# Performance work log

Measured on AMD Instinct MI355X. Metric: run time of the kernel, lower is better.

Reference implementation:

```python
import jax, jax.numpy as jnp
import numpy as np

EPS = 1e-6
H = 8  # num_heads

def setup_inputs() -> dict:
    key = jax.random.key(0)
    ks = jax.random.split(key, 8)
    B, N, M, C, L = 4, 8192, 2048, 512, 256
    s = lambda f_in: 1.0 / np.sqrt(f_in)
    return {
        "input_tokens": jax.random.normal(ks[0], (B, N, C), jnp.float32),
        "query_tokens": jax.random.normal(ks[1], (B, M, C), jnp.float32),
        "Wq": jax.random.normal(ks[2], (C, L), jnp.float32) * s(C),
        "bq": jax.random.normal(ks[3], (L,), jnp.float32) * 0.01,
        "Wk": jax.random.normal(ks[4], (C, L), jnp.float32) * s(C),
        "bk": jax.random.normal(ks[5], (L,), jnp.float32) * 0.01,
        "Wv": jax.random.normal(ks[6], (C, C), jnp.float32) * s(C),
        "bv": jax.random.normal(ks[7], (C,), jnp.float32) * 0.01,
    }

def reference(input_tokens, query_tokens, Wq, bq, Wk, bk, Wv, bv):
    B, N, C = input_tokens.shape
    _, M, _ = query_tokens.shape
    L = Wq.shape[1]
    dL, dC = L // H, C // H
    # projections + head split
    q = (query_tokens @ Wq + bq).reshape(B, M, H, dL)
    k = (input_tokens @ Wk + bk).reshape(B, N, H, dL)
    v = (input_tokens @ Wv + bv).reshape(B, N, H, dC)
    # ELU+1 feature maps (positive kernel)
    q = jax.nn.elu(q) + 1.0
    k = jax.nn.elu(k) + 1.0
    # kv aggregation over input tokens: [B,H,dC,dL]
    kv = jnp.einsum('bnhd,bnhm->bhmd', k, v)
    # normalizer: q . sum_n k  -> [B,M,H]
    z = 1.0 / (jnp.einsum('bmhd,bhd->bmh', q, k.sum(axis=1)) + EPS)
    out = jnp.einsum('bmhd,bhcd,bmh->bmhc', q, kv, z)  # [B,M,H,dC]
    return out.reshape(B, M, C)
```

## Files before the change

### kernel.cpp

```cpp
#include <hip/hip_runtime.h>
#include <hip/hip_bf16.h>
#include <stdint.h>

typedef __bf16 bf16x8 __attribute__((ext_vector_type(8)));
typedef float f32x4 __attribute__((ext_vector_type(4)));

#define GLD16(gp, lp) __builtin_amdgcn_global_load_lds( \
    (__attribute__((address_space(1))) void*)(gp),      \
    (__attribute__((address_space(3))) void*)(lp), 16, 0, 0)

#define Bb 4
#define Nn 8192
#define Mm 2048
#define Cc 512
#define Ll 256
#define Hh 8
#define NTOK 32768

__global__ __launch_bounds__(256) void convert_q(
    const float* __restrict__ Q, __hip_bfloat16* __restrict__ Qb)
{
    long i = ((long)blockIdx.x * 256 + threadIdx.x) * 8;
    float4 a = *(const float4*)(Q + i);
    float4 b = *(const float4*)(Q + i + 4);
    __hip_bfloat16 t8[8] = {
        __float2bfloat16(a.x), __float2bfloat16(a.y),
        __float2bfloat16(a.z), __float2bfloat16(a.w),
        __float2bfloat16(b.x), __float2bfloat16(b.y),
        __float2bfloat16(b.z), __float2bfloat16(b.w)};
    *(uint4*)(Qb + i) = *(const uint4*)t8;
}

__global__ __launch_bounds__(256) void transpose_x(
    const float* __restrict__ X,
    __hip_bfloat16* __restrict__ Xb, __hip_bfloat16* __restrict__ XbT)
{
    __shared__ __hip_bfloat16 ldsT[64][72];
    const int tn = blockIdx.x, tc = blockIdx.y;
    const long n0 = (long)tn * 64;
    const int c0 = tc * 64;
    const int t = threadIdx.x;
    const int rl = t >> 4;
    const int c4 = (t & 15) * 4;
#pragma unroll
    for (int u = 0; u < 4; ++u) {
        const int row = rl + u * 16;
        f32x4 a = *(const f32x4*)(X + (n0 + row) * Cc + c0 + c4);
        __hip_bfloat16 b4[4] = {
            __float2bfloat16(a.x), __float2bfloat16(a.y),
            __float2bfloat16(a.z), __float2bfloat16(a.w)};
        *(ushort2*)(&Xb[(n0 + row) * Cc + c0 + c4]) = *(const ushort2*)b4;
        *(ushort2*)(&Xb[(n0 + row) * Cc + c0 + c4 + 2]) = *(const ushort2*)(b4 + 2);
#pragma unroll
        for (int i = 0; i < 4; ++i) ldsT[c4 + i][row] = b4[i];
    }
    __syncthreads();
#pragma unroll
    for (int u = 0; u < 2; ++u) {
        const int v = u * 256 + t;
        const int orow = v >> 3;
        const int oc8 = (v & 7) * 8;
        bf16x8 r = *(const bf16x8*)(&ldsT[orow][oc8]);
        *(bf16x8*)(&XbT[(long)(c0 + orow) * NTOK + n0 + oc8]) = r;
    }
}

__global__ __launch_bounds__(256) void transpose_w2(
    const float* __restrict__ Wk, const float* __restrict__ Wq,
    __hip_bfloat16* __restrict__ WkT, __hip_bfloat16* __restrict__ WqT)
{
    int idx = blockIdx.x * 256 + threadIdx.x;
    const int NK = 256 * 512;
    if (idx < NK) {
        int j = idx >> 9, c = idx & 511;
        WkT[idx] = __float2bfloat16(Wk[c * 256 + j]);
    } else {
        int k = idx - NK;
        int j = k >> 9, c = k & 511;
        WqT[k] = __float2bfloat16(Wq[c * 256 + j]);
    }
}

template<int MODE>
__global__ __launch_bounds__(256)
void gemm_bt(const __hip_bfloat16* __restrict__ A, long lda,
             const __hip_bfloat16* __restrict__ Bt, long ldb,
             const float* __restrict__ bias,
             void* __restrict__ Cout, long ldc, int Klen)
{
    __shared__ char lds[2][16384];
    const int tid  = threadIdx.x;
    const int lane = tid & 63;
    const int wv   = tid >> 6;
    const int wm   = wv >> 1, wn = wv & 1;
    const long gm0 = (long)blockIdx.x * 128;
    const long gn0 = (long)blockIdx.y * 128;

    long koff_el = 0;
    if (MODE == 2) {
        const int z = blockIdx.z;
        koff_el = (long)(z >> 3) * Nn + (long)(z & 7) * 1024;
    }

    const int o0 = tid * 16;
    const int row0 = o0 >> 6;
    const int kb0 = o0 & 63;
    const int o1 = o0 + 4096;
    const int row1 = row0 + 64;
    const long sA = lda * 2, sB = ldb * 2;
    const char* pA0 = (const char*)A + (gm0 + row0) * sA + koff_el * 2 + kb0;
    const char* pA1 = (const char*)A + (gm0 + row1) * sA + koff_el * 2 + kb0;
    const char* pB0 = (const char*)Bt + (gn0 + row0) * sB + koff_el * 2 + kb0;
    const char* pB1 = (const char*)Bt + (gn0 + row1) * sB + koff_el * 2 + kb0;

    f32x4 acc[4][4];
#pragma unroll
    for (int i = 0; i < 4; i++)
#pragma unroll
        for (int j = 0; j < 4; j++) acc[i][j] = (f32x4){0.f, 0.f, 0.f, 0.f};

    const int l16 = lane & 15, lq = lane >> 4;
    int aoff[4], boff[4];
#pragma unroll
    for (int i = 0; i < 4; i++) {
        aoff[i] = (wm * 64 + i * 16 + l16) * 64 + lq * 16;
        boff[i] = 8192 + (wn * 64 + i * 16 + l16) * 64 + lq * 16;
    }

    const int KT = Klen >> 5;
    {
        char* bf = lds[0];
        GLD16(pA0, bf + o0); GLD16(pA1, bf + o1);
        GLD16(pB0, bf + 8192 + o0); GLD16(pB1, bf + 8192 + o1);
    }
    __syncthreads();
    for (int kt = 0; kt < KT; ++kt) {
        const int cur = kt & 1;
        if (kt + 1 < KT) {
            char* bf = lds[cur ^ 1];
            const long kb = (long)(kt + 1) * 64;
            GLD16(pA0 + kb, bf + o0); GLD16(pA1 + kb, bf + o1);
            GLD16(pB0 + kb, bf + 8192 + o0); GLD16(pB1 + kb, bf + 8192 + o1);
        }
        const char* lp = lds[cur];
        bf16x8 af[4], bfr[4];
#pragma unroll
        for (int i = 0; i < 4; i++) af[i]  = *(const bf16x8*)(lp + aoff[i]);
#pragma unroll
        for (int j = 0; j < 4; j++) bfr[j] = *(const bf16x8*)(lp + boff[j]);
#pragma unroll
        for (int i = 0; i < 4; i++)
#pragma unroll
            for (int j = 0; j < 4; j++)
                acc[i][j] = __builtin_amdgcn_mfma_f32_16x16x32_bf16(
                    af[i], bfr[j], acc[i][j], 0, 0, 0);
        __syncthreads();
    }

    __hip_bfloat16* Cb = (__hip_bfloat16*)Cout;
    float* Cf = (float*)Cout;
    if (MODE == 2) Cf += (long)blockIdx.z * (512 * 256);
#pragma unroll
    for (int i = 0; i < 4; i++) {
        const long gmr = gm0 + wm * 64 + i * 16 + lq * 4;
#pragma unroll
        for (int j = 0; j < 4; j++) {
            const int gn = (int)gn0 + wn * 64 + j * 16 + l16;
#pragma unroll
            for (int v = 0; v < 4; v++) {
                float x = acc[i][j][v];
                if (MODE == 0) {
                    x += bias[gmr + v];
                    x = (x > 0.f) ? x + 1.f : __expf(x);
                    Cb[(gmr + v) * ldc + gn] = __float2bfloat16(x);
                } else if (MODE == 1) {
                    x += bias[gn];
                    x = (x > 0.f) ? x + 1.f : __expf(x);
                    Cb[(gmr + v) * ldc + gn] = __float2bfloat16(x);
                } else {
                    Cf[(gmr + v) * ldc + gn] = x;
                }
            }
        }
    }
}

__global__ __launch_bounds__(256)
void ksum_kernel(const __hip_bfloat16* __restrict__ kT, float* __restrict__ ksum)
{
    const int j = blockIdx.x;
    const int b = blockIdx.y;
    const int t = threadIdx.x;
    const __hip_bfloat16* row = kT + (long)j * NTOK + b * Nn + t * 32;
    float s = 0.f;
#pragma unroll
    for (int u = 0; u < 4; ++u) {
        bf16x8 kv8 = *(const bf16x8*)(row + u * 8);
#pragma unroll
        for (int e = 0; e < 8; ++e) s += (float)kv8[e];
    }
    __shared__ float red[256];
    red[t] = s;
    __syncthreads();
    for (int st = 128; st > 0; st >>= 1) {
        if (t < st) red[t] += red[t + st];
        __syncthreads();
    }
    if (t == 0) ksum[b * 256 + j] = red[0];
}

__global__ __launch_bounds__(256)
void reduce_xk(const float* __restrict__ part, float* __restrict__ xk)
{
    int idx = blockIdx.x * 256 + threadIdx.x;
    int b = idx >> 17, r = idx & 131071;
    const float* p = part + (long)b * 8 * 131072 + r;
    float s = 0.f;
#pragma unroll
    for (int ks = 0; ks < 8; ++ks) s += p[(long)ks * 131072];
    xk[idx] = s;
}

__global__ __launch_bounds__(256)
void wv_contract(const float* __restrict__ xk, const float* __restrict__ Wv,
                 const float* __restrict__ bv, const float* __restrict__ ksum,
                 float* __restrict__ kvagg)
{
    __shared__ float xs[512][32];
    const int chg = blockIdx.x;
    const int b = blockIdx.y;
    const int t = threadIdx.x;
    const int ch0 = chg * 16;
    const int h = ch0 >> 6;
    const float* xb = xk + (long)b * 131072 + h * 32;
#pragma unroll
    for (int u = 0; u < 16; ++u) {
        const int v = u * 256 + t;
        const int row = v >> 3, c4 = (v & 7) * 4;
        *(f32x4*)&xs[row][c4] = *(const f32x4*)&xb[(long)row * 256 + c4];
    }
    __syncthreads();
    const int ch_l = t >> 4;
    const int d0 = (t & 15) * 2;
    const int ch = ch0 + ch_l;
    float a0 = 0.f, a1 = 0.f;
#pragma unroll 8
    for (int c = 0; c < 512; ++c) {
        const float w = Wv[(long)c * 512 + ch];
        a0 = fmaf(w, xs[c][d0], a0);
        a1 = fmaf(w, xs[c][d0 + 1], a1);
    }
    const float bvv = bv[ch];
    const float* ks = ksum + b * 256 + h * 32;
    a0 += bvv * ks[d0];
    a1 += bvv * ks[d0 + 1];
    float* op = kvagg + (((long)(b * 8 + h) * 64 + (ch & 63)) * 32);
    op[d0] = a0;
    op[d0 + 1] = a1;
}

__global__ __launch_bounds__(256)
void z_kernel(const __hip_bfloat16* __restrict__ qb,
              const float* __restrict__ ksum, float* __restrict__ zb)
{
    int t = blockIdx.x * 256 + threadIdx.x;
    int m = t >> 3, h = t & 7;
    int b = m >> 11;
    const __hip_bfloat16* q = qb + (long)m * 256 + h * 32;
    const float* ks = ksum + ((long)b * Hh + h) * 32;
    float s = 0.f;
#pragma unroll
    for (int d8 = 0; d8 < 4; ++d8) {
        bf16x8 qv = *(const bf16x8*)(q + d8 * 8);
#pragma unroll
        for (int u = 0; u < 8; ++u) s = fmaf((float)qv[u], ks[d8 * 8 + u], s);
    }
    zb[t] = 1.f / (s + 1e-6f);
}

__global__ __launch_bounds__(256)
void out_kernel(const __hip_bfloat16* __restrict__ qb,
                const float* __restrict__ kvagg, const float* __restrict__ zb,
                float* __restrict__ out)
{
    __shared__ float lqf[32 * 256];
    __shared__ float lz[32 * 8];
    const int b = blockIdx.y, mt = blockIdx.x;
    const int t = threadIdx.x;
    const long qrow0 = (long)b * Mm + mt * 32;

#pragma unroll
    for (int r = 0; r < 4; ++r) {
        int e = (r * 256 + t) * 8;
        bf16x8 qv = *(const bf16x8*)(qb + qrow0 * 256 + e);
        f32x4 lo = {(float)qv[0], (float)qv[1], (float)qv[2], (float)qv[3]};
        f32x4 hi = {(float)qv[4], (float)qv[5], (float)qv[6], (float)qv[7]};
        *(f32x4*)&lqf[e] = lo;
        *(f32x4*)&lqf[e + 4] = hi;
    }
    lz[t] = zb[qrow0 * 8 + t];

    float kv0[32], kv1[32];
    const float* kvb = kvagg + (long)b * (Hh * 64 * 32);
#pragma unroll
    for (int d4 = 0; d4 < 8; ++d4) {
        *(f32x4*)&kv0[d4 * 4] = *(const f32x4*)&kvb[(long)t * 32 + d4 * 4];
        *(f32x4*)&kv1[d4 * 4] = *(const f32x4*)&kvb[((long)t + 256) * 32 + d4 * 4];
    }
    __syncthreads();

    const int h0 = t >> 6;
    for (int r = 0; r < 32; ++r) {
        float a0 = 0.f, a1 = 0.f;
        const float* q0 = &lqf[r * 256 + h0 * 32];
        const float* q1 = q0 + 128;
#pragma unroll
        for (int d = 0; d < 32; ++d) {
            a0 = fmaf(q0[d], kv0[d], a0);
            a1 = fmaf(q1[d], kv1[d], a1);
        }
        const float z0 = lz[r * 8 + h0];
        const float z1 = lz[r * 8 + h0 + 4];
        const long ob = (qrow0 + r) * 512;
        out[ob + t] = a0 * z0;
        out[ob + t + 256] = a1 * z1;
    }
}

extern "C" void kernel_launch(void* const* d_in, const int* in_sizes, int n_in,
                              void* d_out, int out_size, void* d_ws, size_t ws_size,
                              hipStream_t stream)
{
    const float* X  = (const float*)d_in[0];
    const float* Qt = (const float*)d_in[1];
    const float* Wq = (const float*)d_in[2];
    const float* bq = (const float*)d_in[3];
    const float* Wk = (const float*)d_in[4];
    const float* bk = (const float*)d_in[5];
    const float* Wv = (const float*)d_in[6];
    const float* bv = (const float*)d_in[7];
    float* out = (float*)d_out;

    __hip_bfloat16* Xb    = (__hip_bfloat16*)d_ws;
    __hip_bfloat16* Qb    = Xb + (long)NTOK * Cc;
    __hip_bfloat16* XbT   = Qb + (long)8192 * Cc;
    __hip_bfloat16* kT    = XbT + (long)Cc * NTOK;
    __hip_bfloat16* WkT   = kT + (long)Ll * NTOK;
    __hip_bfloat16* WqT   = WkT + 256 * 512;
    __hip_bfloat16* qbuf  = WqT + 256 * 512;
    float* xk    = (float*)(qbuf + (long)8192 * 256);
    float* kvagg = xk + (long)4 * 512 * 256;
    float* ksum  = kvagg + 4 * 8 * 64 * 32;
    float* zbuf  = ksum + 4 * 256;
    float* xkpart = (float*)d_ws;

    convert_q<<<2048, 256, 0, stream>>>(Qt, Qb);
    transpose_x<<<dim3(512, 8), 256, 0, stream>>>(X, Xb, XbT);
    transpose_w2<<<1024, 256, 0, stream>>>(Wk, Wq, WkT, WqT);
    gemm_bt<0><<<dim3(2, 256), 256, 0, stream>>>(WkT, 512, Xb, 512, bk, kT, NTOK, 512);
    gemm_bt<1><<<dim3(64, 2), 256, 0, stream>>>(Qb, 512, WqT, 512, bq, qbuf, 256, 512);
    ksum_kernel<<<dim3(256, 4), 256, 0, stream>>>(kT, ksum);
    gemm_bt<2><<<dim3(4, 2, 32), 256, 0, stream>>>(XbT, NTOK, kT, NTOK, nullptr, xkpart, 256, 1024);
    reduce_xk<<<2048, 256, 0, stream>>>(xkpart, xk);
    wv_contract<<<dim3(32, 4), 256, 0, stream>>>(xk, Wv, bv, ksum, kvagg);
    z_kernel<<<256, 256, 0, stream>>>(qbuf, ksum, zbuf);
    out_kernel<<<dim3(64, 4), 256, 0, stream>>>(qbuf, kvagg, zbuf, out);
}
```

Measured before the change: 241.3 us.

## Fuse projection GEMMs, fold ksum into K epilogue, merge z into output kernel

Merges the Q-convert and weight-transpose kernels into one prep launch, and runs the K and Q projection GEMMs in a single launch. The key-sum reduction moves into the K GEMM epilogue using wave shuffles and atomics, which removes a separate pass over kT. The XᵀK GEMM split-K goes from 8 to 16 chunks for more blocks, at the cost of a larger partial-reduce. Wv is staged through LDS in wv_contract, the z normalizer is computed inside the output kernel, and the X transpose keeps fp32 in LDS. The changes cut launch count and redundant memory traffic, but add atomics and a memset.

```diff
diff --git a/kernel.cpp b/kernel.cpp
--- a/kernel.cpp
+++ b/kernel.cpp
@@ -17,25 +17,37 @@
 #define Hh 8
 #define NTOK 32768
 
-__global__ __launch_bounds__(256) void convert_q(
-    const float* __restrict__ Q, __hip_bfloat16* __restrict__ Qb)
-{
-    long i = ((long)blockIdx.x * 256 + threadIdx.x) * 8;
-    float4 a = *(const float4*)(Q + i);
-    float4 b = *(const float4*)(Q + i + 4);
-    __hip_bfloat16 t8[8] = {
-        __float2bfloat16(a.x), __float2bfloat16(a.y),
-        __float2bfloat16(a.z), __float2bfloat16(a.w),
-        __float2bfloat16(b.x), __float2bfloat16(b.y),
-        __float2bfloat16(b.z), __float2bfloat16(b.w)};
-    *(uint4*)(Qb + i) = *(const uint4*)t8;
+__global__ __launch_bounds__(256) void prep(
+    const float* __restrict__ Q, const float* __restrict__ Wk,
+    const float* __restrict__ Wq,
+    __hip_bfloat16* __restrict__ Qb, __hip_bfloat16* __restrict__ WkT,
+    __hip_bfloat16* __restrict__ WqT)
+{
+    const int bid = blockIdx.x;
+    if (bid < 2048) {
+        long i = ((long)bid * 256 + threadIdx.x) * 8;
+        float4 a = *(const float4*)(Q + i);
+        float4 b = *(const float4*)(Q + i + 4);
+        __hip_bfloat16 t8[8] = {
+            __float2bfloat16(a.x), __float2bfloat16(a.y),
+            __float2bfloat16(a.z), __float2bfloat16(a.w),
+            __float2bfloat16(b.x), __float2bfloat16(b.y),
+            __float2bfloat16(b.z), __float2bfloat16(b.w)};
+        *(uint4*)(Qb + i) = *(const uint4*)t8;
+    } else {
+        int idx = (bid - 2048) * 256 + threadIdx.x;
+        int k = idx & 131071;
+        int j = k >> 9, c = k & 511;
+        if (idx < 131072) WkT[k] = __float2bfloat16(Wk[c * 256 + j]);
+        else              WqT[k] = __float2bfloat16(Wq[c * 256 + j]);
+    }
 }
 
 __global__ __launch_bounds__(256) void transpose_x(
     const float* __restrict__ X,
     __hip_bfloat16* __restrict__ Xb, __hip_bfloat16* __restrict__ XbT)
 {
-    __shared__ __hip_bfloat16 ldsT[64][72];
+    __shared__ float lt[64][65];
     const int tn = blockIdx.x, tc = blockIdx.y;
     const long n0 = (long)tn * 64;
     const int c0 = tc * 64;
@@ -49,44 +61,151 @@
         __hip_bfloat16 b4[4] = {
             __float2bfloat16(a.x), __float2bfloat16(a.y),
             __float2bfloat16(a.z), __float2bfloat16(a.w)};
-        *(ushort2*)(&Xb[(n0 + row) * Cc + c0 + c4]) = *(const ushort2*)b4;
-        *(ushort2*)(&Xb[(n0 + row) * Cc + c0 + c4 + 2]) = *(const ushort2*)(b4 + 2);
-#pragma unroll
-        for (int i = 0; i < 4; ++i) ldsT[c4 + i][row] = b4[i];
+        *(ushort4*)(&Xb[(n0 + row) * Cc + c0 + c4]) = *(const ushort4*)b4;
+        lt[c4 + 0][row] = a.x; lt[c4 + 1][row] = a.y;
+        lt[c4 + 2][row] = a.z; lt[c4 + 3][row] = a.w;
     }
     __syncthreads();
 #pragma unroll
     for (int u = 0; u < 2; ++u) {
         const int v = u * 256 + t;
-        const int orow = v >> 3;
-        const int oc8 = (v & 7) * 8;
-        bf16x8 r = *(const bf16x8*)(&ldsT[orow][oc8]);
-        *(bf16x8*)(&XbT[(long)(c0 + orow) * NTOK + n0 + oc8]) = r;
-    }
-}
-
-__global__ __launch_bounds__(256) void transpose_w2(
-    const float* __restrict__ Wk, const float* __restrict__ Wq,
-    __hip_bfloat16* __restrict__ WkT, __hip_bfloat16* __restrict__ WqT)
-{
-    int idx = blockIdx.x * 256 + threadIdx.x;
-    const int NK = 256 * 512;
-    if (idx < NK) {
-        int j = idx >> 9, c = idx & 511;
-        WkT[idx] = __float2bfloat16(Wk[c * 256 + j]);
+        const int c = v >> 3;
+        const int n8 = (v & 7) * 8;
+        __hip_bfloat16 o8[8];
+#pragma unroll
+        for (int j = 0; j < 8; ++j) o8[j] = __float2bfloat16(lt[c][n8 + j]);
+        *(uint4*)(&XbT[(long)(c0 + c) * NTOK + n0 + n8]) = *(const uint4*)o8;
+    }
+}
+
+__global__ __launch_bounds__(256)
+void gemm_proj(const __hip_bfloat16* __restrict__ WkT,
+               const __hip_bfloat16* __restrict__ Xb,
+               const __hip_bfloat16* __restrict__ Qb,
+               const __hip_bfloat16* __restrict__ WqT,
+               const float* __restrict__ bk, const float* __restrict__ bq,
+               __hip_bfloat16* __restrict__ kT, __hip_bfloat16* __restrict__ qbuf,
+               float* __restrict__ ksum)
+{
+    __shared__ char lds[2][16384];
+    const bool isK = blockIdx.x < 512;
+    const __hip_bfloat16 *A, *B;
+    long gm0, gn0;
+    if (isK) {
+        const int bid = blockIdx.x;
+        gm0 = (long)(bid & 1) * 128;
+        gn0 = (long)(bid >> 1) * 128;
+        A = WkT; B = Xb;
     } else {
-        int k = idx - NK;
-        int j = k >> 9, c = k & 511;
-        WqT[k] = __float2bfloat16(Wq[c * 256 + j]);
-    }
-}
-
-template<int MODE>
+        const int b2 = blockIdx.x - 512;
+        gm0 = (long)(b2 >> 1) * 128;
+        gn0 = (long)(b2 & 1) * 128;
+        A = Qb; B = WqT;
+    }
+    const int tid  = threadIdx.x;
+    const int lane = tid & 63;
+    const int wv   = tid >> 6;
+    const int wm   = wv >> 1, wn = wv & 1;
+
+    const int o0 = tid * 16;
+    const int row0 = o0 >> 6;
+    const int kb0 = o0 & 63;
+    const int o1 = o0 + 4096;
+    const int row1 = row0 + 64;
+    const char* pA0 = (const char*)A + (gm0 + row0) * 1024 + kb0;
+    const char* pA1 = (const char*)A + (gm0 + row1) * 1024 + kb0;
+    const char* pB0 = (const char*)B + (gn0 + row0) * 1024 + kb0;
+    const char* pB1 = (const char*)B + (gn0 + row1) * 1024 + kb0;
+
+    f32x4 acc[4][4];
+#pragma unroll
+    for (int i = 0; i < 4; i++)
+#pragma unroll
+        for (int j = 0; j < 4; j++) acc[i][j] = (f32x4){0.f, 0.f, 0.f, 0.f};
+
+    const int l16 = lane & 15, lq = lane >> 4;
+    int aoff[4], boff[4];
+#pragma unroll
+    for (int i = 0; i < 4; i++) {
+        aoff[i] = (wm * 64 + i * 16 + l16) * 64 + lq * 16;
+        boff[i] = 8192 + (wn * 64 + i * 16 + l16) * 64 + lq * 16;
+    }
+
+    {
+        char* bf = lds[0];
+        GLD16(pA0, bf + o0); GLD16(pA1, bf + o1);
+        GLD16(pB0, bf + 8192 + o0); GLD16(pB1, bf + 8192 + o1);
+    }
+    __syncthreads();
+#pragma unroll 1
+    for (int kt = 0; kt < 16; ++kt) {
+        const int cur = kt & 1;
+        if (kt + 1 < 16) {
+            char* bf = lds[cur ^ 1];
+            const long kb = (long)(kt + 1) * 64;
+            GLD16(pA0 + kb, bf + o0); GLD16(pA1 + kb, bf + o1);
+            GLD16(pB0 + kb, bf + 8192 + o0); GLD16(pB1 + kb, bf + 8192 + o1);
+        }
+        const char* lp = lds[cur];
+        bf16x8 af[4], bfr[4];
+#pragma unroll
+        for (int i = 0; i < 4; i++) af[i]  = *(const bf16x8*)(lp + aoff[i]);
+#pragma unroll
+        for (int j = 0; j < 4; j++) bfr[j] = *(const bf16x8*)(lp + boff[j]);
+#pragma unroll
+        for (int i = 0; i < 4; i++)
+#pragma unroll
+            for (int j = 0; j < 4; j++)
+                acc[i][j] = __builtin_amdgcn_mfma_f32_16x16x32_bf16(
+                    af[i], bfr[j], acc[i][j], 0, 0, 0);
+        __syncthreads();
+    }
+
+    if (isK) {
+        const int batch = (int)(gn0 >> 13);
+#pragma unroll
+        for (int i = 0; i < 4; i++) {
+            const long gmr = gm0 + wm * 64 + i * 16 + lq * 4;
+#pragma unroll
+            for (int v = 0; v < 4; v++) {
+                const float bias = bk[gmr + v];
+                float s = 0.f;
+#pragma unroll
+                for (int j = 0; j < 4; j++) {
+                    const int gn = (int)gn0 + wn * 64 + j * 16 + l16;
+                    float x = acc[i][j][v] + bias;
+                    x = (x > 0.f) ? x + 1.f : __expf(x);
+                    kT[gmr * NTOK + (long)v * NTOK + gn] = __float2bfloat16(x);
+                    s += x;
+                }
+                s += __shfl_xor(s, 1); s += __shfl_xor(s, 2);
+                s += __shfl_xor(s, 4); s += __shfl_xor(s, 8);
+                if (l16 == 0) atomicAdd(&ksum[batch * 256 + gmr + v], s);
+            }
+        }
+    } else {
+#pragma unroll
+        for (int i = 0; i < 4; i++) {
+            const long gmr = gm0 + wm * 64 + i * 16 + lq * 4;
+#pragma unroll
+            for (int j = 0; j < 4; j++) {
+                const int gn = (int)gn0 + wn * 64 + j * 16 + l16;
+                const float bias = bq[gn];
+#pragma unroll
+                for (int v = 0; v < 4; v++) {
+                    float x = acc[i][j][v] + bias;
+                    x = (x > 0.f) ? x + 1.f : __expf(x);
+                    qbuf[(gmr + v) * 256 + gn] = __float2bfloat16(x);
+                }
+            }
+        }
+    }
+}
+
 __global__ __launch_bounds__(256)
-void gemm_bt(const __hip_bfloat16* __restrict__ A, long lda,
-             const __hip_bfloat16* __restrict__ Bt, long ldb,
-             const float* __restrict__ bias,
-             void* __restrict__ Cout, long ldc, int Klen)
+void gemm_xk(const __hip_bfloat16* __restrict__ XbT,
+             const __hip_bfloat16* __restrict__ kT,
+             float* __restrict__ xkpart)
 {
     __shared__ char lds[2][16384];
     const int tid  = threadIdx.x;
@@ -95,23 +214,19 @@
     const int wm   = wv >> 1, wn = wv & 1;
     const long gm0 = (long)blockIdx.x * 128;
     const long gn0 = (long)blockIdx.y * 128;
-
-    long koff_el = 0;
-    if (MODE == 2) {
-        const int z = blockIdx.z;
-        koff_el = (long)(z >> 3) * Nn + (long)(z & 7) * 1024;
-    }
+    const int z = blockIdx.z;
+    const long koff = (long)(z >> 4) * Nn + (long)(z & 15) * 512;
 
     const int o0 = tid * 16;
     const int row0 = o0 >> 6;
     const int kb0 = o0 & 63;
     const int o1 = o0 + 4096;
     const int row1 = row0 + 64;
-    const long sA = lda * 2, sB = ldb * 2;
-    const char* pA0 = (const char*)A + (gm0 + row0) * sA + koff_el * 2 + kb0;
-    const char* pA1 = (const char*)A + (gm0 + row1) * sA + koff_el * 2 + kb0;
-    const char* pB0 = (const char*)Bt + (gn0 + row0) * sB + koff_el * 2 + kb0;
-    const char* pB1 = (const char*)Bt + (gn0 + row1) * sB + koff_el * 2 + kb0;
+    const long sR = (long)NTOK * 2;
+    const char* pA0 = (const char*)XbT + (gm0 + row0) * sR + koff * 2 + kb0;
+    const char* pA1 = (const char*)XbT + (gm0 + row1) * sR + koff * 2 + kb0;
+    const char* pB0 = (const char*)kT + (gn0 + row0) * sR + koff * 2 + kb0;
+    const char* pB1 = (const char*)kT + (gn0 + row1) * sR + koff * 2 + kb0;
 
     f32x4 acc[4][4];
 #pragma unroll
@@ -127,16 +242,16 @@
         boff[i] = 8192 + (wn * 64 + i * 16 + l16) * 64 + lq * 16;
     }
 
-    const int KT = Klen >> 5;
     {
         char* bf = lds[0];
         GLD16(pA0, bf + o0); GLD16(pA1, bf + o1);
         GLD16(pB0, bf + 8192 + o0); GLD16(pB1, bf + 8192 + o1);
     }
     __syncthreads();
-    for (int kt = 0; kt < KT; ++kt) {
+#pragma unroll 1
+    for (int kt = 0; kt < 16; ++kt) {
         const int cur = kt & 1;
-        if (kt + 1 < KT) {
+        if (kt + 1 < 16) {
             char* bf = lds[cur ^ 1];
             const long kb = (long)(kt + 1) * 64;
             GLD16(pA0 + kb, bf + o0); GLD16(pA1 + kb, bf + o1);
@@ -157,9 +272,7 @@
         __syncthreads();
     }
 
-    __hip_bfloat16* Cb = (__hip_bfloat16*)Cout;
-    float* Cf = (float*)Cout;
-    if (MODE == 2) Cf += (long)blockIdx.z * (512 * 256);
+    float* Cf = xkpart + (long)z * 131072;
 #pragma unroll
     for (int i = 0; i < 4; i++) {
         const long gmr = gm0 + wm * 64 + i * 16 + lq * 4;
@@ -167,46 +280,10 @@
         for (int j = 0; j < 4; j++) {
             const int gn = (int)gn0 + wn * 64 + j * 16 + l16;
 #pragma unroll
-            for (int v = 0; v < 4; v++) {
-                float x = acc[i][j][v];
-                if (MODE == 0) {
-                    x += bias[gmr + v];
-                    x = (x > 0.f) ? x + 1.f : __expf(x);
-                    Cb[(gmr + v) * ldc + gn] = __float2bfloat16(x);
-                } else if (MODE == 1) {
-                    x += bias[gn];
-                    x = (x > 0.f) ? x + 1.f : __expf(x);
-                    Cb[(gmr + v) * ldc + gn] = __float2bfloat16(x);
-                } else {
-                    Cf[(gmr + v) * ldc + gn] = x;
-                }
-            }
-        }
-    }
-}
-
-__global__ __launch_bounds__(256)
-void ksum_kernel(const __hip_bfloat16* __restrict__ kT, float* __restrict__ ksum)
-{
-    const int j = blockIdx.x;
-    const int b = blockIdx.y;
-    const int t = threadIdx.x;
-    const __hip_bfloat16* row = kT + (long)j * NTOK + b * Nn + t * 32;
-    float s = 0.f;
-#pragma unroll
-    for (int u = 0; u < 4; ++u) {
-        bf16x8 kv8 = *(const bf16x8*)(row + u * 8);
-#pragma unroll
-        for (int e = 0; e < 8; ++e) s += (float)kv8[e];
-    }
-    __shared__ float red[256];
-    red[t] = s;
-    __syncthreads();
-    for (int st = 128; st > 0; st >>= 1) {
-        if (t < st) red[t] += red[t + st];
-        __syncthreads();
-    }
-    if (t == 0) ksum[b * 256 + j] = red[0];
+            for (int v = 0; v < 4; v++)
+                Cf[(gmr + v) * 256 + gn] = acc[i][j][v];
+        }
+    }
 }
 
 __global__ __launch_bounds__(256)
@@ -214,10 +291,10 @@
 {
     int idx = blockIdx.x * 256 + threadIdx.x;
     int b = idx >> 17, r = idx & 131071;
-    const float* p = part + (long)b * 8 * 131072 + r;
+    const float* p = part + (long)b * 16 * 131072 + r;
     float s = 0.f;
 #pragma unroll
-    for (int ks = 0; ks < 8; ++ks) s += p[(long)ks * 131072];
+    for (int ks = 0; ks < 16; ++ks) s += p[(long)ks * 131072];
     xk[idx] = s;
 }
 
@@ -227,6 +304,7 @@
                  float* __restrict__ kvagg)
 {
     __shared__ float xs[512][32];
+    __shared__ float wvs[512][16];
     const int chg = blockIdx.x;
     const int b = blockIdx.y;
     const int t = threadIdx.x;
@@ -236,8 +314,14 @@
 #pragma unroll
     for (int u = 0; u < 16; ++u) {
         const int v = u * 256 + t;
-        const int row = v >> 3, c4 = (v & 7) * 4;
-        *(f32x4*)&xs[row][c4] = *(const f32x4*)&xb[(long)row * 256 + c4];
+        const int row = v >> 3, cq = (v & 7) * 4;
+        *(f32x4*)&xs[row][cq] = *(const f32x4*)&xb[(long)row * 256 + cq];
+    }
+#pragma unroll
+    for (int u = 0; u < 8; ++u) {
+        const int v = u * 256 + t;
+        const int row = v >> 2, q = (v & 3) * 4;
+        *(f32x4*)&wvs[row][q] = *(const f32x4*)&Wv[(long)row * 512 + ch0 + q];
     }
     __syncthreads();
     const int ch_l = t >> 4;
@@ -246,7 +330,7 @@
     float a0 = 0.f, a1 = 0.f;
 #pragma unroll 8
     for (int c = 0; c < 512; ++c) {
-        const float w = Wv[(long)c * 512 + ch];
+        const float w = wvs[c][ch_l];
         a0 = fmaf(w, xs[c][d0], a0);
         a1 = fmaf(w, xs[c][d0 + 1], a1);
     }
@@ -260,31 +344,13 @@
 }
 
 __global__ __launch_bounds__(256)
-void z_kernel(const __hip_bfloat16* __restrict__ qb,
-              const float* __restrict__ ksum, float* __restrict__ zb)
-{
-    int t = blockIdx.x * 256 + threadIdx.x;
-    int m = t >> 3, h = t & 7;
-    int b = m >> 11;
-    const __hip_bfloat16* q = qb + (long)m * 256 + h * 32;
-    const float* ks = ksum + ((long)b * Hh + h) * 32;
-    float s = 0.f;
-#pragma unroll
-    for (int d8 = 0; d8 < 4; ++d8) {
-        bf16x8 qv = *(const bf16x8*)(q + d8 * 8);
-#pragma unroll
-        for (int u = 0; u < 8; ++u) s = fmaf((float)qv[u], ks[d8 * 8 + u], s);
-    }
-    zb[t] = 1.f / (s + 1e-6f);
-}
-
-__global__ __launch_bounds__(256)
-void out_kernel(const __hip_bfloat16* __restrict__ qb,
-                const float* __restrict__ kvagg, const float* __restrict__ zb,
-                float* __restrict__ out)
+void out_z(const __hip_bfloat16* __restrict__ qb,
+           const float* __restrict__ kvagg, const float* __restrict__ ksum,
+           float* __restrict__ out)
 {
     __shared__ float lqf[32 * 256];
-    __shared__ float lz[32 * 8];
+    __shared__ float lks[256];
+    __shared__ float lz[256];
     const int b = blockIdx.y, mt = blockIdx.x;
     const int t = threadIdx.x;
     const long qrow0 = (long)b * Mm + mt * 32;
@@ -298,7 +364,7 @@
         *(f32x4*)&lqf[e] = lo;
         *(f32x4*)&lqf[e + 4] = hi;
     }
-    lz[t] = zb[qrow0 * 8 + t];
+    lks[t] = ksum[b * 256 + t];
 
     float kv0[32], kv1[32];
     const float* kvb = kvagg + (long)b * (Hh * 64 * 32);
@@ -306,6 +372,17 @@
     for (int d4 = 0; d4 < 8; ++d4) {
         *(f32x4*)&kv0[d4 * 4] = *(const f32x4*)&kvb[(long)t * 32 + d4 * 4];
         *(f32x4*)&kv1[d4 * 4] = *(const f32x4*)&kvb[((long)t + 256) * 32 + d4 * 4];
+    }
+    __syncthreads();
+
+    {
+        const int r = t >> 3, h = t & 7;
+        const float* q = &lqf[r * 256 + h * 32];
+        const float* ks = &lks[h * 32];
+        float s = 0.f;
+#pragma unroll
+        for (int d = 0; d < 32; ++d) s = fmaf(q[d], ks[d], s);
+        lz[t] = 1.f / (s + 1e-6f);
     }
     __syncthreads();
 
@@ -351,18 +428,14 @@
     float* xk    = (float*)(qbuf + (long)8192 * 256);
     float* kvagg = xk + (long)4 * 512 * 256;
     float* ksum  = kvagg + 4 * 8 * 64 * 32;
-    float* zbuf  = ksum + 4 * 256;
     float* xkpart = (float*)d_ws;
 
-    convert_q<<<2048, 256, 0, stream>>>(Qt, Qb);
+    hipMemsetAsync(ksum, 0, 4 * 256 * sizeof(float), stream);
+    prep<<<3072, 256, 0, stream>>>(Qt, Wk, Wq, Qb, WkT, WqT);
     transpose_x<<<dim3(512, 8), 256, 0, stream>>>(X, Xb, XbT);
-    transpose_w2<<<1024, 256, 0, stream>>>(Wk, Wq, WkT, WqT);
-    gemm_bt<0><<<dim3(2, 256), 256, 0, stream>>>(WkT, 512, Xb, 512, bk, kT, NTOK, 512);
-    gemm_bt<1><<<dim3(64, 2), 256, 0, stream>>>(Qb, 512, WqT, 512, bq, qbuf, 256, 512);
-    ksum_kernel<<<dim3(256, 4), 256, 0, stream>>>(kT, ksum);
-    gemm_bt<2><<<dim3(4, 2, 32), 256, 0, stream>>>(XbT, NTOK, kT, NTOK, nullptr, xkpart, 256, 1024);
+    gemm_proj<<<640, 256, 0, stream>>>(WkT, Xb, Qb, WqT, bk, bq, kT, qbuf, ksum);
+    gemm_xk<<<dim3(4, 2, 64), 256, 0, stream>>>(XbT, kT, xkpart);
     reduce_xk<<<2048, 256, 0, stream>>>(xkpart, xk);
     wv_contract<<<dim3(32, 4), 256, 0, stream>>>(xk, Wv, bv, ksum, kvagg);
-    z_kernel<<<256, 256, 0, stream>>>(qbuf, ksum, zbuf);
-    out_kernel<<<dim3(64, 4), 256, 0, stream>>>(qbuf, kvagg, zbuf, out);
-}
+    out_z<<<dim3(64, 4), 256, 0, stream>>>(qbuf, kvagg, ksum, out);
+}
```

Result: no change. 238.9 us (-1.0%).
